# Kernel optimization log

Hardware: AMD Instinct MI355X
Metric: run time of the kernel (lower is better)

Reference implementation:

```python
import jax, jax.numpy as jnp
import numpy as np

EPS = 1e-6
B, H, S, D = 8, 16, 4096, 64


def setup_inputs() -> dict:
    key = jax.random.key(0)
    k1, k2, k3 = jax.random.split(key, 3)
    return {
        "keys": jax.random.normal(k1, (B, H, S, D), dtype=jnp.float32),
        "values": jax.random.normal(k2, (B, H, S, D), dtype=jnp.float32),
        "queries": jax.random.normal(k3, (B, H, S, D), dtype=jnp.float32),
    }


def reference(keys, values, queries):
    # update: accumulate outer-product associative memory per (batch, head)
    # M[b,h] = sum_s k_s outer v_s  -> [B, H, D, D]
    M = jnp.einsum("bhsd,bhse->bhde", keys, values)
    # normalizer z[b,h] = sum_s k_s -> [B, H, D]
    z = jnp.sum(keys, axis=2)
    # retrieve: out = (q @ M) / (q . z + eps)
    num = jnp.einsum("bhqd,bhde->bhqe", queries, M)        # [B, H, S, D]
    den = jnp.einsum("bhqd,bhd->bhq", queries, z) + EPS     # [B, H, S]
    return num / den[..., None]
```

## Files before the change

### kernel.cpp

```cpp
#include <hip/hip_runtime.h>

constexpr int Sc = 4096, Dc = 64;
constexpr int BH = 128;
constexpr int SS = 8;
constexpr int CHUNK = Sc / SS;
constexpr int SROWS = 32;
constexpr int NST = CHUNK / SROWS;
constexpr int MM = Dc * Dc;
constexpr int LSTR = 66;
constexpr int NZC = SS * SROWS;
constexpr int QT = 128;

using sh8 = __attribute__((ext_vector_type(8))) short;
using f32x4 = __attribute__((ext_vector_type(4))) float;

__device__ __forceinline__ unsigned int packbf2(float lo, float hi) {
  unsigned int a = __builtin_bit_cast(unsigned int, lo);
  unsigned int b = __builtin_bit_cast(unsigned int, hi);
  a = (a + 0x7fffu + ((a >> 16) & 1u)) >> 16;
  b = (b + 0x7fffu + ((b >> 16) & 1u)) & 0xffff0000u;
  return a | b;
}

__global__ __launch_bounds__(256) void k1_accum(const float* __restrict__ K,
                                                const float* __restrict__ V,
                                                float* __restrict__ Pm,
                                                double* __restrict__ Pz) {
  const int blk = blockIdx.x, bh = blk >> 3, ck = blk & 7;
  const int tid = threadIdx.x, w = tid >> 6, l = tid & 63;
  const int g = l >> 4, c = l & 15;
  const int s_l = tid >> 3, dblk = tid & 7;

  const size_t base = ((size_t)bh * Sc + (size_t)ck * CHUNK) * Dc;
  const float4* gk4 = (const float4*)(K + base);
  const float4* gv4 = (const float4*)(V + base);
  const int ldi = s_l * 16 + dblk * 2;

  __shared__ __align__(16) unsigned short lk[2][SROWS * LSTR];
  __shared__ __align__(16) unsigned short lv[2][SROWS * LSTR];

  f32x4 acc[4];
  #pragma unroll
  for (int i = 0; i < 4; ++i) acc[i] = (f32x4){0.f, 0.f, 0.f, 0.f};
  double zacc[8] = {};

  float4 ka, kb, va, vb;

#define K1_STAGEWRITE(BUF)                                                   \
  {                                                                          \
    unsigned int* dk = (unsigned int*)&lk[BUF][s_l * LSTR + dblk * 8];       \
    dk[0] = packbf2(ka.x, ka.y); dk[1] = packbf2(ka.z, ka.w);                \
    dk[2] = packbf2(kb.x, kb.y); dk[3] = packbf2(kb.z, kb.w);                \
    unsigned int* dv = (unsigned int*)&lv[BUF][s_l * LSTR + dblk * 8];       \
    dv[0] = packbf2(va.x, va.y); dv[1] = packbf2(va.z, va.w);                \
    dv[2] = packbf2(vb.x, vb.y); dv[3] = packbf2(vb.z, vb.w);                \
    zacc[0] += (double)ka.x; zacc[1] += (double)ka.y;                        \
    zacc[2] += (double)ka.z; zacc[3] += (double)ka.w;                        \
    zacc[4] += (double)kb.x; zacc[5] += (double)kb.y;                        \
    zacc[6] += (double)kb.z; zacc[7] += (double)kb.w;                        \
  }

  ka = gk4[ldi]; kb = gk4[ldi + 1]; va = gv4[ldi]; vb = gv4[ldi + 1];
  K1_STAGEWRITE(0)
  __syncthreads();

  for (int st = 0; st < NST; ++st) {
    const int cur = st & 1;
    if (st + 1 < NST) {
      const int o = (st + 1) * (SROWS * 16);
      ka = gk4[o + ldi]; kb = gk4[o + ldi + 1];
      va = gv4[o + ldi]; vb = gv4[o + ldi + 1];
    }
    const unsigned short* plk = lk[cur];
    const unsigned short* plv = lv[cur];
    sh8 afr;
    #pragma unroll
    for (int j = 0; j < 8; ++j)
      afr[j] = (short)plk[(8 * g + j) * LSTR + 16 * w + c];
    #pragma unroll
    for (int et = 0; et < 4; ++et) {
      sh8 bfr;
      #pragma unroll
      for (int j = 0; j < 8; ++j)
        bfr[j] = (short)plv[(8 * g + j) * LSTR + 16 * et + c];
      acc[et] = __builtin_amdgcn_mfma_f32_16x16x32_bf16(afr, bfr, acc[et], 0, 0, 0);
    }
    if (st + 1 < NST) {
      K1_STAGEWRITE((st + 1) & 1)
    }
    __syncthreads();
  }
#undef K1_STAGEWRITE

  float* pd = Pm + ((size_t)ck * BH + bh) * MM;
  #pragma unroll
  for (int et = 0; et < 4; ++et)
    #pragma unroll
    for (int r = 0; r < 4; ++r)
      pd[(16 * w + 4 * g + r) * 64 + 16 * et + c] = acc[et][r];

  double* pz = Pz + ((size_t)ck * SROWS + s_l) * (size_t)(BH * 64) +
               (size_t)bh * 64 + dblk * 8;
  #pragma unroll
  for (int j = 0; j < 8; ++j) pz[j] = zacc[j];
}

__global__ __launch_bounds__(256) void k2_reduce(const float* __restrict__ Pm,
                                                 const double* __restrict__ Pz,
                                                 float* __restrict__ Fm,
                                                 float* __restrict__ Fz) {
  const int i = blockIdx.x * 256 + threadIdx.x;
  const int nm = BH * MM;
  if (i < nm) {
    float s = 0.f;
    #pragma unroll
    for (int cc = 0; cc < SS; ++cc) s += Pm[(size_t)cc * nm + i];
    Fm[i] = s;
  }
  const int nz = BH * Dc;
  if (i < nz) {
    double s = 0.0;
    for (int cc = 0; cc < NZC; ++cc) s += Pz[(size_t)cc * nz + i];
    Fz[i] = (float)s;
  }
}

__global__ __launch_bounds__(256) void k3_retrieve(const float* __restrict__ Q,
                                                   const float* __restrict__ Fm,
                                                   const float* __restrict__ Fz,
                                                   float* __restrict__ O) {
  const int blk = blockIdx.x;
  const int bh = blk >> 5;
  const int row0 = (blk & 31) * QT;

  __shared__ __align__(16) float lm[Dc][Dc];
  __shared__ __align__(16) float lq[QT][68];
  __shared__ __align__(16) float lz[Dc];

  const int tid = threadIdx.x;

  const float4* gm4 = (const float4*)(Fm + (size_t)bh * MM);
  float4* lm4 = (float4*)&lm[0][0];
  #pragma unroll
  for (int j = 0; j < 4; ++j) lm4[tid + j * 256] = gm4[tid + j * 256];
  if (tid < Dc) lz[tid] = Fz[(size_t)bh * Dc + tid];

  const float4* gq4 = (const float4*)(Q + ((size_t)bh * Sc + row0) * Dc);
  #pragma unroll
  for (int j = 0; j < 8; ++j) {
    const int i4 = tid + j * 256;
    const float4 v = gq4[i4];
    const int f = i4 * 4;
    *(float4*)&lq[f >> 6][f & 63] = v;
  }
  __syncthreads();

  const int rg = tid >> 3;
  const int cg = tid & 7;
  const int r0 = rg * 4;
  const int e0 = cg * 8;

  float acc[4][8] = {};
  double den[4] = {0.0, 0.0, 0.0, 0.0};

  #pragma unroll
  for (int ds = 0; ds < 16; ++ds) {
    const int d0 = ds * 4;
    const float4 z4 = *(const float4*)&lz[d0];
    const float* zf = (const float*)&z4;
    float4 q4[4];
    #pragma unroll
    for (int r = 0; r < 4; ++r) q4[r] = *(const float4*)&lq[r0 + r][d0];
    const float* qf[4] = {(const float*)&q4[0], (const float*)&q4[1],
                          (const float*)&q4[2], (const float*)&q4[3]};
    #pragma unroll
    for (int i = 0; i < 4; ++i) {
      const float4 ma = *(const float4*)&lm[d0 + i][e0];
      const float4 mb = *(const float4*)&lm[d0 + i][e0 + 4];
      const float mf[8] = {ma.x, ma.y, ma.z, ma.w, mb.x, mb.y, mb.z, mb.w};
      const double zd = (double)zf[i];
      #pragma unroll
      for (int r = 0; r < 4; ++r) {
        const float qs = qf[r][i];
        den[r] += (double)qs * zd;
        #pragma unroll
        for (int j = 0; j < 8; ++j)
          acc[r][j] = fmaf(qs, mf[j], acc[r][j]);
      }
    }
  }

  #pragma unroll
  for (int r = 0; r < 4; ++r) {
    const double iv = 1.0 / (den[r] + 1e-6);
    float* go = O + ((size_t)bh * Sc + row0 + r0 + r) * Dc + e0;
    ((float4*)go)[0] = make_float4((float)((double)acc[r][0] * iv),
                                   (float)((double)acc[r][1] * iv),
                                   (float)((double)acc[r][2] * iv),
                                   (float)((double)acc[r][3] * iv));
    ((float4*)go)[1] = make_float4((float)((double)acc[r][4] * iv),
                                   (float)((double)acc[r][5] * iv),
                                   (float)((double)acc[r][6] * iv),
                                   (float)((double)acc[r][7] * iv));
  }
}

extern "C" void kernel_launch(void* const* d_in, const int* in_sizes, int n_in,
                              void* d_out, int out_size, void* d_ws, size_t ws_size,
                              hipStream_t stream) {
  const float* K = (const float*)d_in[0];
  const float* V = (const float*)d_in[1];
  const float* Q = (const float*)d_in[2];
  float* O = (float*)d_out;

  float* Pm = (float*)d_ws;
  float* Fm = Pm + (size_t)SS * BH * MM;
  double* Pz = (double*)(Fm + (size_t)BH * MM);
  float* Fz = (float*)(Pz + (size_t)NZC * BH * Dc);

  hipLaunchKernelGGL(k1_accum, dim3(BH * SS), dim3(256), 0, stream, K, V, Pm, Pz);
  hipLaunchKernelGGL(k2_reduce, dim3((BH * MM + 255) / 256), dim3(256), 0, stream, Pm, Pz, Fm, Fz);
  hipLaunchKernelGGL(k3_retrieve, dim3(BH * (Sc / QT)), dim3(256), 0, stream, Q, Fm, Fz, O);
}
```

Measured before the change: 173.5 us.

## Deepen k1 global-load prefetch to three stages ahead with register rotation

The accumulate kernel now keeps four register sets of K/V tiles and issues each global load three stages before it is written to LDS, instead of one stage ahead. The loop is unrolled by four so the register sets rotate statically. This aims to hide global memory latency in the load-bound accumulate phase. In exchange it raises register pressure, which could lower occupancy.

```diff
diff --git a/kernel.cpp b/kernel.cpp
--- a/kernel.cpp
+++ b/kernel.cpp
@@ -44,53 +44,75 @@
   for (int i = 0; i < 4; ++i) acc[i] = (f32x4){0.f, 0.f, 0.f, 0.f};
   double zacc[8] = {};
 
-  float4 ka, kb, va, vb;
-
-#define K1_STAGEWRITE(BUF)                                                   \
+  float4 k0a, k0b, v0a, v0b, k1a, k1b, v1a, v1b;
+  float4 k2a, k2b, v2a, v2b, k3a, k3b, v3a, v3b;
+
+#define K1_LOADSET(KA, KB, VA, VB, ST)                                       \
+  {                                                                          \
+    const int o_ = (ST) * (SROWS * 16);                                      \
+    KA = gk4[o_ + ldi]; KB = gk4[o_ + ldi + 1];                              \
+    VA = gv4[o_ + ldi]; VB = gv4[o_ + ldi + 1];                              \
+  }
+
+#define K1_WRITESET(KA, KB, VA, VB, BUF)                                     \
   {                                                                          \
     unsigned int* dk = (unsigned int*)&lk[BUF][s_l * LSTR + dblk * 8];       \
-    dk[0] = packbf2(ka.x, ka.y); dk[1] = packbf2(ka.z, ka.w);                \
-    dk[2] = packbf2(kb.x, kb.y); dk[3] = packbf2(kb.z, kb.w);                \
+    dk[0] = packbf2(KA.x, KA.y); dk[1] = packbf2(KA.z, KA.w);                \
+    dk[2] = packbf2(KB.x, KB.y); dk[3] = packbf2(KB.z, KB.w);                \
     unsigned int* dv = (unsigned int*)&lv[BUF][s_l * LSTR + dblk * 8];       \
-    dv[0] = packbf2(va.x, va.y); dv[1] = packbf2(va.z, va.w);                \
-    dv[2] = packbf2(vb.x, vb.y); dv[3] = packbf2(vb.z, vb.w);                \
-    zacc[0] += (double)ka.x; zacc[1] += (double)ka.y;                        \
-    zacc[2] += (double)ka.z; zacc[3] += (double)ka.w;                        \
-    zacc[4] += (double)kb.x; zacc[5] += (double)kb.y;                        \
-    zacc[6] += (double)kb.z; zacc[7] += (double)kb.w;                        \
-  }
-
-  ka = gk4[ldi]; kb = gk4[ldi + 1]; va = gv4[ldi]; vb = gv4[ldi + 1];
-  K1_STAGEWRITE(0)
+    dv[0] = packbf2(VA.x, VA.y); dv[1] = packbf2(VA.z, VA.w);                \
+    dv[2] = packbf2(VB.x, VB.y); dv[3] = packbf2(VB.z, VB.w);                \
+    zacc[0] += (double)KA.x; zacc[1] += (double)KA.y;                        \
+    zacc[2] += (double)KA.z; zacc[3] += (double)KA.w;                        \
+    zacc[4] += (double)KB.x; zacc[5] += (double)KB.y;                        \
+    zacc[6] += (double)KB.z; zacc[7] += (double)KB.w;                        \
+  }
+
+#define K1_COMPUTE(BUF)                                                      \
+  {                                                                          \
+    const unsigned short* plk = lk[BUF];                                     \
+    const unsigned short* plv = lv[BUF];                                     \
+    sh8 afr;                                                                 \
+    _Pragma("unroll")                                                        \
+    for (int j = 0; j < 8; ++j)                                              \
+      afr[j] = (short)plk[(8 * g + j) * LSTR + 16 * w + c];                  \
+    _Pragma("unroll")                                                        \
+    for (int et = 0; et < 4; ++et) {                                         \
+      sh8 bfr;                                                               \
+      _Pragma("unroll")                                                      \
+      for (int j = 0; j < 8; ++j)                                            \
+        bfr[j] = (short)plv[(8 * g + j) * LSTR + 16 * et + c];               \
+      acc[et] = __builtin_amdgcn_mfma_f32_16x16x32_bf16(afr, bfr, acc[et], 0, 0, 0); \
+    }                                                                        \
+  }
+
+  K1_LOADSET(k0a, k0b, v0a, v0b, 0)
+  K1_LOADSET(k1a, k1b, v1a, v1b, 1)
+  K1_LOADSET(k2a, k2b, v2a, v2b, 2)
+  K1_WRITESET(k0a, k0b, v0a, v0b, 0)
   __syncthreads();
 
-  for (int st = 0; st < NST; ++st) {
-    const int cur = st & 1;
-    if (st + 1 < NST) {
-      const int o = (st + 1) * (SROWS * 16);
-      ka = gk4[o + ldi]; kb = gk4[o + ldi + 1];
-      va = gv4[o + ldi]; vb = gv4[o + ldi + 1];
-    }
-    const unsigned short* plk = lk[cur];
-    const unsigned short* plv = lv[cur];
-    sh8 afr;
-    #pragma unroll
-    for (int j = 0; j < 8; ++j)
-      afr[j] = (short)plk[(8 * g + j) * LSTR + 16 * w + c];
-    #pragma unroll
-    for (int et = 0; et < 4; ++et) {
-      sh8 bfr;
-      #pragma unroll
-      for (int j = 0; j < 8; ++j)
-        bfr[j] = (short)plv[(8 * g + j) * LSTR + 16 * et + c];
-      acc[et] = __builtin_amdgcn_mfma_f32_16x16x32_bf16(afr, bfr, acc[et], 0, 0, 0);
-    }
-    if (st + 1 < NST) {
-      K1_STAGEWRITE((st + 1) & 1)
-    }
-    __syncthreads();
-  }
-#undef K1_STAGEWRITE
+  for (int stb = 0; stb < NST; stb += 4) {
+    if (stb + 3 < NST) K1_LOADSET(k3a, k3b, v3a, v3b, stb + 3)
+    K1_COMPUTE(0)
+    if (stb + 1 < NST) K1_WRITESET(k1a, k1b, v1a, v1b, 1)
+    __syncthreads();
+    if (stb + 4 < NST) K1_LOADSET(k0a, k0b, v0a, v0b, stb + 4)
+    K1_COMPUTE(1)
+    if (stb + 2 < NST) K1_WRITESET(k2a, k2b, v2a, v2b, 0)
+    __syncthreads();
+    if (stb + 5 < NST) K1_LOADSET(k1a, k1b, v1a, v1b, stb + 5)
+    K1_COMPUTE(0)
+    if (stb + 3 < NST) K1_WRITESET(k3a, k3b, v3a, v3b, 1)
+    __syncthreads();
+    if (stb + 6 < NST) K1_LOADSET(k2a, k2b, v2a, v2b, stb + 6)
+    K1_COMPUTE(1)
+    if (stb + 4 < NST) K1_WRITESET(k0a, k0b, v0a, v0b, 0)
+    __syncthreads();
+  }
+#undef K1_LOADSET
+#undef K1_WRITESET
+#undef K1_COMPUTE
 
   float* pd = Pm + ((size_t)ck * BH + bh) * MM;
   #pragma unroll
```

After: 177.4 us. +2.2%, slower.

## Load K/V MFMA fragments straight from global memory, dropping LDS staging

Applied to the files above, without the earlier changes.

The accumulate kernel no longer stages K and V through double-buffered shared memory with barriers. Each lane now loads its MFMA fragment elements directly from global memory as strided scalar loads, packs them to bf16 in registers, and accumulates the key-sum per lane. This cuts the z partials from 256 to 32 per head, which shrinks the reduce loop. In exchange, the global loads are uncoalesced scalar loads (each lane reads one float per row), and V elements are read by all four waves redundantly, so memory efficiency may suffer.

```diff
diff --git a/kernel.cpp b/kernel.cpp
--- a/kernel.cpp
+++ b/kernel.cpp
@@ -7,8 +7,7 @@
 constexpr int SROWS = 32;
 constexpr int NST = CHUNK / SROWS;
 constexpr int MM = Dc * Dc;
-constexpr int LSTR = 66;
-constexpr int NZC = SS * SROWS;
+constexpr int NZP = SS * 4;
 constexpr int QT = 128;
 
 using sh8 = __attribute__((ext_vector_type(8))) short;
@@ -29,68 +28,46 @@
   const int blk = blockIdx.x, bh = blk >> 3, ck = blk & 7;
   const int tid = threadIdx.x, w = tid >> 6, l = tid & 63;
   const int g = l >> 4, c = l & 15;
-  const int s_l = tid >> 3, dblk = tid & 7;
 
   const size_t base = ((size_t)bh * Sc + (size_t)ck * CHUNK) * Dc;
-  const float4* gk4 = (const float4*)(K + base);
-  const float4* gv4 = (const float4*)(V + base);
-  const int ldi = s_l * 16 + dblk * 2;
-
-  __shared__ __align__(16) unsigned short lk[2][SROWS * LSTR];
-  __shared__ __align__(16) unsigned short lv[2][SROWS * LSTR];
+  const float* kcol = K + base + 16 * w + c;
+  const float* vcol = V + base + c;
 
   f32x4 acc[4];
   #pragma unroll
   for (int i = 0; i < 4; ++i) acc[i] = (f32x4){0.f, 0.f, 0.f, 0.f};
-  double zacc[8] = {};
-
-  float4 ka, kb, va, vb;
-
-#define K1_STAGEWRITE(BUF)                                                   \
-  {                                                                          \
-    unsigned int* dk = (unsigned int*)&lk[BUF][s_l * LSTR + dblk * 8];       \
-    dk[0] = packbf2(ka.x, ka.y); dk[1] = packbf2(ka.z, ka.w);                \
-    dk[2] = packbf2(kb.x, kb.y); dk[3] = packbf2(kb.z, kb.w);                \
-    unsigned int* dv = (unsigned int*)&lv[BUF][s_l * LSTR + dblk * 8];       \
-    dv[0] = packbf2(va.x, va.y); dv[1] = packbf2(va.z, va.w);                \
-    dv[2] = packbf2(vb.x, vb.y); dv[3] = packbf2(vb.z, vb.w);                \
-    zacc[0] += (double)ka.x; zacc[1] += (double)ka.y;                        \
-    zacc[2] += (double)ka.z; zacc[3] += (double)ka.w;                        \
-    zacc[4] += (double)kb.x; zacc[5] += (double)kb.y;                        \
-    zacc[6] += (double)kb.z; zacc[7] += (double)kb.w;                        \
-  }
-
-  ka = gk4[ldi]; kb = gk4[ldi + 1]; va = gv4[ldi]; vb = gv4[ldi + 1];
-  K1_STAGEWRITE(0)
-  __syncthreads();
+  double zacc = 0.0;
 
   for (int st = 0; st < NST; ++st) {
-    const int cur = st & 1;
-    if (st + 1 < NST) {
-      const int o = (st + 1) * (SROWS * 16);
-      ka = gk4[o + ldi]; kb = gk4[o + ldi + 1];
-      va = gv4[o + ldi]; vb = gv4[o + ldi + 1];
-    }
-    const unsigned short* plk = lk[cur];
-    const unsigned short* plv = lv[cur];
-    sh8 afr;
+    const int rowf = (st * SROWS + 8 * g) * Dc;
+
+    float ak[8];
     #pragma unroll
-    for (int j = 0; j < 8; ++j)
-      afr[j] = (short)plk[(8 * g + j) * LSTR + 16 * w + c];
+    for (int j = 0; j < 8; ++j) ak[j] = kcol[rowf + j * Dc];
+
+    float bv[4][8];
+    #pragma unroll
+    for (int et = 0; et < 4; ++et)
+      #pragma unroll
+      for (int j = 0; j < 8; ++j) bv[et][j] = vcol[rowf + j * Dc + 16 * et];
+
+    #pragma unroll
+    for (int j = 0; j < 8; ++j) zacc += (double)ak[j];
+
+    unsigned int au[4];
+    #pragma unroll
+    for (int j = 0; j < 4; ++j) au[j] = packbf2(ak[2 * j], ak[2 * j + 1]);
+    const sh8 afr = __builtin_bit_cast(sh8, *(const uint4*)au);
+
     #pragma unroll
     for (int et = 0; et < 4; ++et) {
-      sh8 bfr;
+      unsigned int bu[4];
       #pragma unroll
-      for (int j = 0; j < 8; ++j)
-        bfr[j] = (short)plv[(8 * g + j) * LSTR + 16 * et + c];
+      for (int j = 0; j < 4; ++j) bu[j] = packbf2(bv[et][2 * j], bv[et][2 * j + 1]);
+      const sh8 bfr = __builtin_bit_cast(sh8, *(const uint4*)bu);
       acc[et] = __builtin_amdgcn_mfma_f32_16x16x32_bf16(afr, bfr, acc[et], 0, 0, 0);
     }
-    if (st + 1 < NST) {
-      K1_STAGEWRITE((st + 1) & 1)
-    }
-    __syncthreads();
   }
-#undef K1_STAGEWRITE
 
   float* pd = Pm + ((size_t)ck * BH + bh) * MM;
   #pragma unroll
@@ -99,10 +76,7 @@
     for (int r = 0; r < 4; ++r)
       pd[(16 * w + 4 * g + r) * 64 + 16 * et + c] = acc[et][r];
 
-  double* pz = Pz + ((size_t)ck * SROWS + s_l) * (size_t)(BH * 64) +
-               (size_t)bh * 64 + dblk * 8;
-  #pragma unroll
-  for (int j = 0; j < 8; ++j) pz[j] = zacc[j];
+  Pz[((size_t)(ck * 4 + g) * BH + bh) * Dc + 16 * w + c] = zacc;
 }
 
 __global__ __launch_bounds__(256) void k2_reduce(const float* __restrict__ Pm,
@@ -120,7 +94,8 @@
   const int nz = BH * Dc;
   if (i < nz) {
     double s = 0.0;
-    for (int cc = 0; cc < NZC; ++cc) s += Pz[(size_t)cc * nz + i];
+    #pragma unroll
+    for (int cc = 0; cc < NZP; ++cc) s += Pz[(size_t)cc * nz + i];
     Fz[i] = (float)s;
   }
 }
@@ -216,7 +191,7 @@
   float* Pm = (float*)d_ws;
   float* Fm = Pm + (size_t)SS * BH * MM;
   double* Pz = (double*)(Fm + (size_t)BH * MM);
-  float* Fz = (float*)(Pz + (size_t)NZC * BH * Dc);
+  float* Fz = (float*)(Pz + (size_t)NZP * BH * Dc);
 
   hipLaunchKernelGGL(k1_accum, dim3(BH * SS), dim3(256), 0, stream, K, V, Pm, Pz);
   hipLaunchKernelGGL(k2_reduce, dim3((BH * MM + 255) / 256), dim3(256), 0, stream, Pm, Pz, Fm, Fz);
```

Measured after the change: 169.0 us. 2.6% less time.
